# Kernel tuning notes

Measured on AMD Instinct MI355X. Metric: run time of the kernel, lower is better.

The kernel has to match this reference:

```python
import jax, jax.numpy as jnp
import numpy as np

EMBED_DIM = 1024
N_HEADS = 16
HEAD_DIM = EMBED_DIM // N_HEADS


def setup_inputs() -> dict:
    key = jax.random.key(0)
    k_x, k_qw, k_qb, k_ow, k_ob = jax.random.split(key, 5)
    s = 1.0 / np.sqrt(EMBED_DIM)
    return {
        "x": jax.random.normal(k_x, (2, 2048, EMBED_DIM), dtype=jnp.float32),
        "qkv_w": jax.random.uniform(k_qw, (3 * EMBED_DIM, EMBED_DIM), jnp.float32, -s, s),
        "qkv_b": jax.random.uniform(k_qb, (3 * EMBED_DIM,), jnp.float32, -s, s),
        "out_w": jax.random.uniform(k_ow, (EMBED_DIM, EMBED_DIM), jnp.float32, -s, s),
        "out_b": jax.random.uniform(k_ob, (EMBED_DIM,), jnp.float32, -s, s),
    }


def reference(x, qkv_w, qkv_b, out_w, out_b):
    B, S, E = x.shape
    # fused QKV projection (torch Linear: x @ W^T + b)
    qkv = x @ qkv_w.T + qkv_b                      # [B,S,3E]
    qkv = qkv.reshape(B, S, N_HEADS, 3 * HEAD_DIM).transpose(0, 2, 1, 3)  # [B,H,S,3d]
    q, k, v = jnp.split(qkv, 3, axis=-1)           # each [B,H,S,d]
    scores = jnp.einsum("bhqd,bhkd->bhqk", q, k) / jnp.sqrt(jnp.float32(HEAD_DIM))
    weights = jax.nn.softmax(scores, axis=-1)      # [B,H,S,S]
    attn = jnp.einsum("bhqk,bhkd->bhqd", weights, v)
    attn = attn.transpose(0, 2, 1, 3).reshape(B, S, E)
    return attn @ out_w.T + out_b
```

## Files before the change

kernel.cpp:

```cpp
#include <hip/hip_runtime.h>
#include <hip/hip_bf16.h>


#define E_DIM   1024
#define NHEADS  16
#define HDIM    64
#define SEQ     2048
#define TOK     4096
#define QKV_DIM 3072
#define QK_STRIDE 2048
#define QSCALE_F 0.18033688011112042f

typedef __attribute__((ext_vector_type(8))) short bf16x8;
typedef __attribute__((ext_vector_type(4))) float f32x4;
typedef __attribute__((ext_vector_type(4))) int   i32x4;
typedef __attribute__((ext_vector_type(2))) int   i32x2;
typedef __attribute__((ext_vector_type(2))) __bf16 bf16x2_t;

#if __has_builtin(__builtin_amdgcn_exp2f)
#define EXP2F(x) __builtin_amdgcn_exp2f(x)
#else
#define EXP2F(x) exp2f(x)
#endif

__device__ __forceinline__ unsigned pack2bf(float a, float b) {
#if __has_builtin(__builtin_amdgcn_cvt_pk_bf16_f32)
    union { bf16x2_t v; unsigned u; } u;
    u.v = __builtin_amdgcn_cvt_pk_bf16_f32(a, b);
    return u.u;
#else
    union { float f; unsigned u; } ua, ub; ua.f = a; ub.f = b;
    unsigned ra = ua.u + 0x7FFF + ((ua.u >> 16) & 1);
    unsigned rb = ub.u + 0x7FFF + ((ub.u >> 16) & 1);
    return (ra >> 16) | (rb & 0xFFFF0000u);
#endif
}

__device__ __forceinline__ unsigned short f2bf(float x) {
    return (unsigned short)(pack2bf(x, x) & 0xFFFFu);
}

__device__ __forceinline__ void load_lds16(const void* g, void* l) {
    __builtin_amdgcn_global_load_lds(
        (const __attribute__((address_space(1))) void*)g,
        (__attribute__((address_space(3))) void*)l, 16, 0, 0);
}

__device__ __forceinline__ bf16x8 lds_read8(const unsigned short* p) {
    union { i32x4 i; bf16x8 b; } u;
    u.i = *(const i32x4*)p;
    return u.b;
}

__device__ __forceinline__ f32x4 mfma16(bf16x8 a, bf16x8 b, f32x4 c) {
    return __builtin_amdgcn_mfma_f32_16x16x32_bf16(a, b, c, 0, 0, 0);
}

__global__ void cast3_kernel(const float* __restrict__ a, unsigned short* __restrict__ oa, int na4,
                             const float* __restrict__ b, unsigned short* __restrict__ ob, int nb4,
                             const float* __restrict__ c, unsigned short* __restrict__ oc) {
    int i = blockIdx.x * blockDim.x + threadIdx.x;
    const float* src; unsigned short* dst; int j;
    if (i < na4)            { src = a; dst = oa; j = i; }
    else if (i < na4 + nb4) { src = b; dst = ob; j = i - na4; }
    else                    { src = c; dst = oc; j = i - na4 - nb4; }
    f32x4 v = ((const f32x4*)src)[j];
    union { i32x2 i2; unsigned u[2]; } o;
    o.u[0] = pack2bf(v.x, v.y);
    o.u[1] = pack2bf(v.z, v.w);
    ((i32x2*)dst)[j] = o.i2;
}

__global__ __launch_bounds__(256, 3)
void gemm_qkv_kernel(const unsigned short* __restrict__ A,
                     const unsigned short* __restrict__ B,
                     const float* __restrict__ bias,
                     unsigned short* __restrict__ qk,
                     unsigned short* __restrict__ vT,
                     int K) {
    __shared__ __align__(16) unsigned short As[128 * 64];
    __shared__ __align__(16) unsigned short Bs[128 * 64];

    const int tid  = threadIdx.x;
    const int wave = tid >> 6, lane = tid & 63;
    const int quad = lane >> 4, l16 = lane & 15;
    const int row0 = blockIdx.y * 128, col0 = blockIdx.x * 128;
    const int wr = (wave >> 1) * 64, wc = (wave & 1) * 64;

    f32x4 acc[4][4];
#pragma unroll
    for (int i = 0; i < 4; ++i)
#pragma unroll
        for (int j = 0; j < 4; ++j) acc[i][j] = (f32x4){0.f, 0.f, 0.f, 0.f};

    const int nkt = K >> 6;
    for (int kt = 0; kt < nkt; ++kt) {
        const int k0 = kt << 6;
#pragma unroll
        for (int i = 0; i < 4; ++i) {
            int p = i * 256 + tid;
            int r = p >> 3;
            int kc = (p & 7) ^ (r & 7);
            load_lds16(A + (size_t)(row0 + r) * K + k0 + kc * 8, &As[p * 8]);
        }
#pragma unroll
        for (int i = 0; i < 4; ++i) {
            int p = i * 256 + tid;
            int r = p >> 3;
            int kc = (p & 7) ^ (r & 7);
            load_lds16(B + (size_t)(col0 + r) * K + k0 + kc * 8, &Bs[p * 8]);
        }
        __syncthreads();

#pragma unroll
        for (int ks = 0; ks < 2; ++ks) {
            bf16x8 af[4], bfr[4];
#pragma unroll
            for (int rb = 0; rb < 4; ++rb) {
                int r_l  = wr + rb * 16 + l16;
                int phys = (ks * 4 + quad) ^ (l16 & 7);
                af[rb] = lds_read8(&As[r_l * 64 + phys * 8]);
            }
#pragma unroll
            for (int cb = 0; cb < 4; ++cb) {
                int r_l  = wc + cb * 16 + l16;
                int phys = (ks * 4 + quad) ^ (l16 & 7);
                bfr[cb] = lds_read8(&Bs[r_l * 64 + phys * 8]);
            }
#pragma unroll
            for (int rb = 0; rb < 4; ++rb)
#pragma unroll
                for (int cb = 0; cb < 4; ++cb)
                    acc[rb][cb] = mfma16(af[rb], bfr[cb], acc[rb][cb]);
        }
        __syncthreads();
    }

#pragma unroll
    for (int rb = 0; rb < 4; ++rb)
#pragma unroll
        for (int cb = 0; cb < 4; ++cb) {
            int col = col0 + wc + cb * 16 + l16;
            int h    = col / 192;
            int part = col - h * 192;
            float bv = bias[col];
            int row_b = row0 + wr + rb * 16 + quad * 4;
            float v[4];
#pragma unroll
            for (int reg = 0; reg < 4; ++reg) v[reg] = acc[rb][cb][reg] + bv;
            if (part < 128) {
                float sc = (part < 64) ? QSCALE_F : 1.0f;
                size_t base = (size_t)h * 128 + part;
#pragma unroll
                for (int reg = 0; reg < 4; ++reg)
                    qk[(size_t)(row_b + reg) * QK_STRIDE + base] = f2bf(v[reg] * sc);
            } else {
                int i  = part - 128;
                int b  = row_b >> 11;
                int s  = row_b & 2047;
                i32x2 pk;
                pk.x = (int)pack2bf(v[0], v[1]);
                pk.y = (int)pack2bf(v[2], v[3]);
                *(i32x2*)&vT[(((size_t)(b * 16 + h)) * 64 + i) * SEQ + s] = pk;
            }
        }
}

__global__ __launch_bounds__(256, 2)
void gemm2_kernel(const unsigned short* __restrict__ A,
                  const unsigned short* __restrict__ B,
                  const float* __restrict__ bias,
                  float* __restrict__ C, int M, int N, int K) {
    __shared__ __align__(16) unsigned short As[128 * 64];
    __shared__ __align__(16) unsigned short Bs[64 * 64];

    const int tid  = threadIdx.x;
    const int wave = tid >> 6, lane = tid & 63;
    const int quad = lane >> 4, l16 = lane & 15;
    const int row0 = blockIdx.y * 128, col0 = blockIdx.x * 64;
    const int wr = wave * 32;

    f32x4 acc[2][4];
#pragma unroll
    for (int i = 0; i < 2; ++i)
#pragma unroll
        for (int j = 0; j < 4; ++j) acc[i][j] = (f32x4){0.f, 0.f, 0.f, 0.f};

    const int nkt = K >> 6;
    for (int kt = 0; kt < nkt; ++kt) {
        const int k0 = kt << 6;
#pragma unroll
        for (int i = 0; i < 4; ++i) {
            int p = i * 256 + tid;
            int r = p >> 3;
            int kc = (p & 7) ^ (r & 7);
            load_lds16(A + (size_t)(row0 + r) * K + k0 + kc * 8, &As[p * 8]);
        }
#pragma unroll
        for (int i = 0; i < 2; ++i) {
            int p = i * 256 + tid;
            int r = p >> 3;
            int kc = (p & 7) ^ (r & 7);
            load_lds16(B + (size_t)(col0 + r) * K + k0 + kc * 8, &Bs[p * 8]);
        }
        __syncthreads();

#pragma unroll
        for (int ks = 0; ks < 2; ++ks) {
            bf16x8 af[2], bfr[4];
#pragma unroll
            for (int rb = 0; rb < 2; ++rb) {
                int r_l  = wr + rb * 16 + l16;
                int phys = (ks * 4 + quad) ^ (l16 & 7);
                af[rb] = lds_read8(&As[r_l * 64 + phys * 8]);
            }
#pragma unroll
            for (int cb = 0; cb < 4; ++cb) {
                int r_l  = cb * 16 + l16;
                int phys = (ks * 4 + quad) ^ (l16 & 7);
                bfr[cb] = lds_read8(&Bs[r_l * 64 + phys * 8]);
            }
#pragma unroll
            for (int rb = 0; rb < 2; ++rb)
#pragma unroll
                for (int cb = 0; cb < 4; ++cb)
                    acc[rb][cb] = mfma16(af[rb], bfr[cb], acc[rb][cb]);
        }
        __syncthreads();
    }

#pragma unroll
    for (int rb = 0; rb < 2; ++rb)
#pragma unroll
        for (int cb = 0; cb < 4; ++cb) {
            int col = col0 + cb * 16 + l16;
            float bv = bias[col];
#pragma unroll
            for (int reg = 0; reg < 4; ++reg) {
                int row = row0 + wr + rb * 16 + quad * 4 + reg;
                C[(size_t)row * N + col] = acc[rb][cb][reg] + bv;
            }
        }
}

__global__ __launch_bounds__(256, 2)
void attn_kernel(const unsigned short* __restrict__ qk,
                 const unsigned short* __restrict__ vT,
                 unsigned short* __restrict__ attn) {
    __shared__ __align__(16) unsigned short lds[24576];

    const int tid  = threadIdx.x;
    const int wave = tid >> 6, lane = tid & 63;
    const int quad = lane >> 4, l16 = lane & 15;
    const int bh = blockIdx.y;
    const int b = bh >> 4, h = bh & 15;
    const int q0 = blockIdx.x * 128;
    const size_t rowbase = (size_t)b * SEQ;
    const int sw3 = l16 & 7;

    const unsigned short* kroot = qk + rowbase * QK_STRIDE + h * 128 + 64;
    const unsigned short* vroot = vT + (size_t)bh * 64 * SEQ;

    int srow[2], scol[2];
#pragma unroll
    for (int i = 0; i < 2; ++i) {
        int p = i * 256 + tid;
        srow[i] = p >> 3;
        scol[i] = ((p & 7) ^ (srow[i] & 7)) * 8;
    }

    const int fO0 = l16 * 64 + ((quad ^ sw3) * 8);
    const int fO1 = l16 * 64 + (((4 + quad) ^ sw3) * 8);
    int pwO[2][4], prO[2][2];
#pragma unroll
    for (int g = 0; g < 2; ++g) {
        int base = 16384 + wave * 2048 + g * 1024;
#pragma unroll
        for (int c4 = 0; c4 < 4; ++c4)
            pwO[g][c4] = base + l16 * 64
                       + (((c4 * 2 + (quad >> 1)) ^ sw3) * 8) + (quad & 1) * 4;
        prO[g][0] = base + fO0;
        prO[g][1] = base + fO1;
    }

    union { short s[8]; bf16x8 v; } uon;
#pragma unroll
    for (int j = 0; j < 8; ++j) uon.s[j] = (short)0x3F80;
    const bf16x8 onesb = uon.v;

    bf16x8 qf[2][2];
#pragma unroll
    for (int g = 0; g < 2; ++g)
#pragma unroll
        for (int ks = 0; ks < 2; ++ks) {
            const unsigned short* p =
                qk + (rowbase + q0 + wave * 32 + g * 16 + l16) * QK_STRIDE
                   + h * 128 + ks * 32 + quad * 8;
            union { i32x4 i; bf16x8 b; } u;
            u.i = *(const i32x4*)p;
            qf[g][ks] = u.b;
        }

    f32x4 o[2][4];
#pragma unroll
    for (int g = 0; g < 2; ++g)
#pragma unroll
        for (int ib = 0; ib < 4; ++ib) o[g][ib] = (f32x4){0.f, 0.f, 0.f, 0.f};
    f32x4 lacc[2];
    lacc[0] = (f32x4){0.f, 0.f, 0.f, 0.f};
    lacc[1] = (f32x4){0.f, 0.f, 0.f, 0.f};

#pragma unroll
    for (int i = 0; i < 2; ++i) {
        int p = i * 256 + tid;
        load_lds16(kroot + srow[i] * QK_STRIDE + scol[i], &lds[p * 8]);
    }
#pragma unroll
    for (int i = 0; i < 2; ++i) {
        int p = i * 256 + tid;
        load_lds16(vroot + srow[i] * SEQ + scol[i], &lds[8192 + p * 8]);
    }

    for (int kt = 0; kt < SEQ / 64; ++kt) {
        const int cur = kt & 1;
        __syncthreads();

        if (kt < SEQ / 64 - 1) {
            const int kb = (kt + 1) * 64;
            const int nb = (cur ^ 1) * 4096;
#pragma unroll
            for (int i = 0; i < 2; ++i) {
                int p = i * 256 + tid;
                load_lds16(kroot + (size_t)(kb + srow[i]) * QK_STRIDE + scol[i],
                           &lds[nb + p * 8]);
            }
#pragma unroll
            for (int i = 0; i < 2; ++i) {
                int p = i * 256 + tid;
                load_lds16(vroot + srow[i] * SEQ + kb + scol[i],
                           &lds[8192 + nb + p * 8]);
            }
        }

        const unsigned short* ksb = &lds[cur * 4096];
        const unsigned short* vsb = &lds[8192 + cur * 4096];

        f32x4 s[2][4];
#pragma unroll
        for (int g = 0; g < 2; ++g)
#pragma unroll
            for (int cb = 0; cb < 4; ++cb) s[g][cb] = (f32x4){0.f, 0.f, 0.f, 0.f};
#pragma unroll
        for (int cb = 0; cb < 4; ++cb) {
            bf16x8 kf = lds_read8(ksb + fO0 + cb * 1024);
            s[0][cb] = mfma16(kf, qf[0][0], s[0][cb]);
            s[1][cb] = mfma16(kf, qf[1][0], s[1][cb]);
        }
#pragma unroll
        for (int cb = 0; cb < 4; ++cb) {
            bf16x8 kf = lds_read8(ksb + fO1 + cb * 1024);
            s[0][cb] = mfma16(kf, qf[0][1], s[0][cb]);
            s[1][cb] = mfma16(kf, qf[1][1], s[1][cb]);
        }

#pragma unroll
        for (int g = 0; g < 2; ++g)
#pragma unroll
            for (int c4 = 0; c4 < 4; ++c4) {
                i32x2 pk;
                pk.x = (int)pack2bf(EXP2F(s[g][c4][0]), EXP2F(s[g][c4][1]));
                pk.y = (int)pack2bf(EXP2F(s[g][c4][2]), EXP2F(s[g][c4][3]));
                *(i32x2*)&lds[pwO[g][c4]] = pk;
            }
        __asm__ volatile("s_waitcnt lgkmcnt(0)" ::: "memory");
        {
            bf16x8 pf[2][2];
#pragma unroll
            for (int g = 0; g < 2; ++g) {
                pf[g][0] = lds_read8(&lds[prO[g][0]]);
                pf[g][1] = lds_read8(&lds[prO[g][1]]);
                lacc[g] = mfma16(pf[g][0], onesb, lacc[g]);
                lacc[g] = mfma16(pf[g][1], onesb, lacc[g]);
            }
#pragma unroll
            for (int ib = 0; ib < 4; ++ib) {
                bf16x8 vf = lds_read8(vsb + fO0 + ib * 1024);
                o[0][ib] = mfma16(pf[0][0], vf, o[0][ib]);
                o[1][ib] = mfma16(pf[1][0], vf, o[1][ib]);
            }
#pragma unroll
            for (int ib = 0; ib < 4; ++ib) {
                bf16x8 vf = lds_read8(vsb + fO1 + ib * 1024);
                o[0][ib] = mfma16(pf[0][1], vf, o[0][ib]);
                o[1][ib] = mfma16(pf[1][1], vf, o[1][ib]);
            }
        }
    }

#pragma unroll
    for (int g = 0; g < 2; ++g) {
        float il[4];
#pragma unroll
        for (int r = 0; r < 4; ++r) il[r] = 1.0f / lacc[g][r];
#pragma unroll
        for (int ib = 0; ib < 4; ++ib)
#pragma unroll
            for (int r = 0; r < 4; ++r) {
                int t = q0 + wave * 32 + g * 16 + quad * 4 + r;
                attn[(rowbase + t) * E_DIM + h * 64 + ib * 16 + l16] =
                    f2bf(o[g][ib][r] * il[r]);
            }
    }
}

extern "C" void kernel_launch(void* const* d_in, const int* in_sizes, int n_in,
                              void* d_out, int out_size, void* d_ws, size_t ws_size,
                              hipStream_t stream) {
    const float* x     = (const float*)d_in[0];
    const float* qkv_w = (const float*)d_in[1];
    const float* qkv_b = (const float*)d_in[2];
    const float* out_w = (const float*)d_in[3];
    const float* out_b = (const float*)d_in[4];

    char* ws = (char*)d_ws;
    unsigned short* xb   = (unsigned short*)(ws);
    unsigned short* wqkv = (unsigned short*)(ws + 8388608);
    unsigned short* wout = (unsigned short*)(ws + 14680064);
    unsigned short* qk   = (unsigned short*)(ws + 16777216);
    unsigned short* attn = (unsigned short*)(ws + 33554432);
    unsigned short* vT   = (unsigned short*)(ws + 41943040);

    cast3_kernel<<<8192, 256, 0, stream>>>(x, xb, 1048576,
                                           qkv_w, wqkv, 786432,
                                           out_w, wout);

    gemm_qkv_kernel<<<dim3(24, 32), 256, 0, stream>>>(
        xb, wqkv, qkv_b, qk, vT, E_DIM);

    attn_kernel<<<dim3(16, 32), 256, 0, stream>>>(qk, vT, attn);

    gemm2_kernel<<<dim3(16, 32), 256, 0, stream>>>(
        attn, wout, out_b, (float*)d_out, TOK, E_DIM, E_DIM);
}
```

Measured before the change: 190.8 us.

## Keep softmax probabilities in registers via permlane swaps instead of LDS round-trip

Replaces the LDS write/read staging of the exponentiated score tile with in-register permlane32/permlane16 swaps that turn the S accumulator layout into the MFMA B-operand layout. The PV and row-sum MFMAs swap operand order, so the output accumulator comes out transposed, and the epilogue now writes packed 4-element bf16 rows. This removes the P staging region from shared memory, shrinking the LDS footprint, and drops an lgkmcnt wait and the LDS traffic in the inner loop. It relies on permlane swap builtins, with a shuffle fallback if they are missing, and on the lane mapping being exactly right.

```diff
diff --git a/kernel.cpp b/kernel.cpp
--- a/kernel.cpp
+++ b/kernel.cpp
@@ -15,6 +15,7 @@
 typedef __attribute__((ext_vector_type(4))) float f32x4;
 typedef __attribute__((ext_vector_type(4))) int   i32x4;
 typedef __attribute__((ext_vector_type(2))) int   i32x2;
+typedef __attribute__((ext_vector_type(2))) unsigned u32x2;
 typedef __attribute__((ext_vector_type(2))) __bf16 bf16x2_t;
 
 #if __has_builtin(__builtin_amdgcn_exp2f)
@@ -38,6 +39,35 @@
 
 __device__ __forceinline__ unsigned short f2bf(float x) {
     return (unsigned short)(pack2bf(x, x) & 0xFFFFu);
+}
+
+__device__ __forceinline__ void pl32swap(unsigned& a, unsigned& b) {
+#if __has_builtin(__builtin_amdgcn_permlane32_swap)
+    u32x2 t = __builtin_amdgcn_permlane32_swap(a, b, false, false);
+    a = t.x; b = t.y;
+#else
+    int lane = (int)(threadIdx.x & 63);
+    unsigned bl = (unsigned)__shfl((int)b, lane - 32);
+    unsigned ah = (unsigned)__shfl((int)a, lane + 32);
+    unsigned na = (lane < 32) ? a : bl;
+    unsigned nb = (lane < 32) ? ah : b;
+    a = na; b = nb;
+#endif
+}
+
+__device__ __forceinline__ void pl16swap(unsigned& a, unsigned& b) {
+#if __has_builtin(__builtin_amdgcn_permlane16_swap)
+    u32x2 t = __builtin_amdgcn_permlane16_swap(a, b, false, false);
+    a = t.x; b = t.y;
+#else
+    int lane = (int)(threadIdx.x & 63);
+    int row  = (lane >> 4) & 3;
+    unsigned bd = (unsigned)__shfl((int)b, lane - 16);
+    unsigned au = (unsigned)__shfl((int)a, lane + 16);
+    unsigned na = (row & 1) ? bd : a;
+    unsigned nb = (row & 1) ? b : au;
+    a = na; b = nb;
+#endif
 }
 
 __device__ __forceinline__ void load_lds16(const void* g, void* l) {
@@ -247,7 +277,7 @@
 void attn_kernel(const unsigned short* __restrict__ qk,
                  const unsigned short* __restrict__ vT,
                  unsigned short* __restrict__ attn) {
-    __shared__ __align__(16) unsigned short lds[24576];
+    __shared__ __align__(16) unsigned short lds[16384];
 
     const int tid  = threadIdx.x;
     const int wave = tid >> 6, lane = tid & 63;
@@ -271,17 +301,6 @@
 
     const int fO0 = l16 * 64 + ((quad ^ sw3) * 8);
     const int fO1 = l16 * 64 + (((4 + quad) ^ sw3) * 8);
-    int pwO[2][4], prO[2][2];
-#pragma unroll
-    for (int g = 0; g < 2; ++g) {
-        int base = 16384 + wave * 2048 + g * 1024;
-#pragma unroll
-        for (int c4 = 0; c4 < 4; ++c4)
-            pwO[g][c4] = base + l16 * 64
-                       + (((c4 * 2 + (quad >> 1)) ^ sw3) * 8) + (quad & 1) * 4;
-        prO[g][0] = base + fO0;
-        prO[g][1] = base + fO1;
-    }
 
     union { short s[8]; bf16x8 v; } uon;
 #pragma unroll
@@ -364,52 +383,47 @@
         }
 
 #pragma unroll
-        for (int g = 0; g < 2; ++g)
-#pragma unroll
-            for (int c4 = 0; c4 < 4; ++c4) {
-                i32x2 pk;
-                pk.x = (int)pack2bf(EXP2F(s[g][c4][0]), EXP2F(s[g][c4][1]));
-                pk.y = (int)pack2bf(EXP2F(s[g][c4][2]), EXP2F(s[g][c4][3]));
-                *(i32x2*)&lds[pwO[g][c4]] = pk;
-            }
-        __asm__ volatile("s_waitcnt lgkmcnt(0)" ::: "memory");
-        {
-            bf16x8 pf[2][2];
+        for (int ks2 = 0; ks2 < 2; ++ks2) {
+            const int c0 = ks2 * 2, c1 = ks2 * 2 + 1;
+            bf16x8 pT[2];
 #pragma unroll
             for (int g = 0; g < 2; ++g) {
-                pf[g][0] = lds_read8(&lds[prO[g][0]]);
-                pf[g][1] = lds_read8(&lds[prO[g][1]]);
-                lacc[g] = mfma16(pf[g][0], onesb, lacc[g]);
-                lacc[g] = mfma16(pf[g][1], onesb, lacc[g]);
-            }
+                unsigned x0a = pack2bf(EXP2F(s[g][c0][0]), EXP2F(s[g][c0][1]));
+                unsigned x1a = pack2bf(EXP2F(s[g][c0][2]), EXP2F(s[g][c0][3]));
+                unsigned x0b = pack2bf(EXP2F(s[g][c1][0]), EXP2F(s[g][c1][1]));
+                unsigned x1b = pack2bf(EXP2F(s[g][c1][2]), EXP2F(s[g][c1][3]));
+                pl32swap(x0a, x0b);
+                pl16swap(x0a, x0b);
+                pl32swap(x1a, x1b);
+                pl16swap(x1a, x1b);
+                union { unsigned u[4]; bf16x8 v; } r;
+                r.u[0] = x0a; r.u[1] = x1a; r.u[2] = x0b; r.u[3] = x1b;
+                pT[g] = r.v;
+            }
+            lacc[0] = mfma16(onesb, pT[0], lacc[0]);
+            lacc[1] = mfma16(onesb, pT[1], lacc[1]);
+            const int fO = ks2 ? fO1 : fO0;
 #pragma unroll
             for (int ib = 0; ib < 4; ++ib) {
-                bf16x8 vf = lds_read8(vsb + fO0 + ib * 1024);
-                o[0][ib] = mfma16(pf[0][0], vf, o[0][ib]);
-                o[1][ib] = mfma16(pf[1][0], vf, o[1][ib]);
-            }
-#pragma unroll
-            for (int ib = 0; ib < 4; ++ib) {
-                bf16x8 vf = lds_read8(vsb + fO1 + ib * 1024);
-                o[0][ib] = mfma16(pf[0][1], vf, o[0][ib]);
-                o[1][ib] = mfma16(pf[1][1], vf, o[1][ib]);
+                bf16x8 vf = lds_read8(vsb + fO + ib * 1024);
+                o[0][ib] = mfma16(vf, pT[0], o[0][ib]);
+                o[1][ib] = mfma16(vf, pT[1], o[1][ib]);
             }
         }
     }
 
 #pragma unroll
     for (int g = 0; g < 2; ++g) {
-        float il[4];
-#pragma unroll
-        for (int r = 0; r < 4; ++r) il[r] = 1.0f / lacc[g][r];
-#pragma unroll
-        for (int ib = 0; ib < 4; ++ib)
-#pragma unroll
-            for (int r = 0; r < 4; ++r) {
-                int t = q0 + wave * 32 + g * 16 + quad * 4 + r;
-                attn[(rowbase + t) * E_DIM + h * 64 + ib * 16 + l16] =
-                    f2bf(o[g][ib][r] * il[r]);
-            }
+        float il = 1.0f / lacc[g][0];
+        int t = q0 + wave * 32 + g * 16 + l16;
+        unsigned short* orow = attn + (rowbase + t) * E_DIM + h * 64 + quad * 4;
+#pragma unroll
+        for (int ib = 0; ib < 4; ++ib) {
+            i32x2 pk;
+            pk.x = (int)pack2bf(o[g][ib][0] * il, o[g][ib][1] * il);
+            pk.y = (int)pack2bf(o[g][ib][2] * il, o[g][ib][3] * il);
+            *(i32x2*)(orow + ib * 16) = pk;
+        }
     }
 }
 
```

Result: faster. 184.9 us (-3.1%).
